# Kernel tuning notes

Measured on AMD Instinct MI355X. Metric: run time of the kernel, lower is better.

Reference implementation:

```python
import jax, jax.numpy as jnp
import numpy as np

B, T, F, U, L = 64, 700, 3, 400, 3


def setup_inputs() -> dict:
    key = jax.random.key(0)
    ks = jax.random.split(key, 10)
    s = 0.08  # small init to keep gates unsaturated
    return {
        "x": jax.random.normal(ks[0], (B, T, F), jnp.float32),
        "Wx0": jax.random.normal(ks[1], (F, 4 * U), jnp.float32) * s,
        "Wx1": jax.random.normal(ks[2], (U, 4 * U), jnp.float32) * s,
        "Wx2": jax.random.normal(ks[3], (U, 4 * U), jnp.float32) * s,
        "Wh": jax.random.normal(ks[4], (L, U, 4 * U), jnp.float32) * s,
        "b": jnp.zeros((L, 4 * U), jnp.float32),
        "pi": jax.random.normal(ks[5], (L, U), jnp.float32) * s,
        "pf": jax.random.normal(ks[6], (L, U), jnp.float32) * s,
        "po": jax.random.normal(ks[7], (L, U), jnp.float32) * s,
        "Wd": jax.random.normal(ks[8], (U, F), jnp.float32) * s,
        "bd": jnp.zeros((F,), jnp.float32),
    }


def _lstm_peephole_layer(x_tbd, Wx, Wh_l, b_l, pi_l, pf_l, po_l):
    """x_tbd: [T, B, D] -> [T, B, U] with peephole LSTM (Graves 2013)."""
    Bsz = x_tbd.shape[1]
    Uu = Wh_l.shape[0]
    # Precompute the input contribution for all timesteps in one GEMM.
    xp = jnp.einsum("tbd,dk->tbk", x_tbd, Wx) + b_l  # [T, B, 4U]

    def step(carry, zt):
        h, c = carry
        z = zt + h @ Wh_l  # [B, 4U]
        zi, zf, zg, zo = jnp.split(z, 4, axis=-1)
        i = jax.nn.sigmoid(zi + pi_l * c)
        f = jax.nn.sigmoid(zf + pf_l * c)
        c_new = f * c + i * jnp.tanh(zg)
        o = jax.nn.sigmoid(zo + po_l * c_new)
        h_new = o * jnp.tanh(c_new)
        return (h_new, c_new), h_new

    init = (jnp.zeros((Bsz, Uu), x_tbd.dtype), jnp.zeros((Bsz, Uu), x_tbd.dtype))
    _, hs = jax.lax.scan(step, init, xp)
    return hs  # [T, B, U]


def reference(x, Wx0, Wx1, Wx2, Wh, b, pi, pf, po, Wd, bd):
    h = jnp.transpose(x, (1, 0, 2))  # [T, B, F]
    for l, Wx in enumerate((Wx0, Wx1, Wx2)):
        h = _lstm_peephole_layer(h, Wx, Wh[l], b[l], pi[l], pf[l], po[l])
    out = jnp.einsum("tbu,uf->tbf", h, Wd) + bd
    return jnp.transpose(out, (1, 0, 2))  # [B, T, F]
```

## Files before the change

### kernel.cpp

```cpp
#include <hip/hip_runtime.h>
#include <hip/hip_fp16.h>
#include <math.h>

#define B_ 64
#define T_ 700
#define U_ 400
#define NF 704
#define FR_LS 13312

typedef _Float16 half8 __attribute__((ext_vector_type(8)));
typedef float float4v __attribute__((ext_vector_type(4)));

union AFrag { unsigned u[4]; half8 h; };

__device__ __forceinline__ unsigned agloadu(const unsigned* p) {
    return __hip_atomic_load(p, __ATOMIC_RELAXED, __HIP_MEMORY_SCOPE_AGENT);
}
__device__ __forceinline__ void agstoreu(unsigned* p, unsigned v) {
    __hip_atomic_store(p, v, __ATOMIC_RELAXED, __HIP_MEMORY_SCOPE_AGENT);
}
__device__ __forceinline__ float sig_(float v) {
    return __builtin_amdgcn_rcpf(1.f + __expf(-v));
}
__device__ __forceinline__ float tanh_(float v) {
    return 1.f - 2.f * __builtin_amdgcn_rcpf(__expf(2.f * v) + 1.f);
}
__device__ __forceinline__ void waitflag(const unsigned* f, unsigned target) {
    while (agloadu(f) < target) __builtin_amdgcn_s_sleep(2);
}
__device__ __forceinline__ unsigned f16u(float v) {
    union { _Float16 f; unsigned short s; } cv; cv.f = (_Float16)v; return (unsigned)cv.s;
}

__device__ __forceinline__ void pollfrag13(const unsigned* __restrict__ base,
                                           const unsigned par,
                                           AFrag* __restrict__ a, const int lane)
{
    {
        const unsigned* pp = base + (lane % 13) * 256 + ((lane * 37) & 255);
        while (!__all((int)(((agloadu(pp) ^ par) & 1u) == 0u)))
            __builtin_amdgcn_s_sleep(3);
    }
    unsigned pend = 0x1FFFu;
    do {
#pragma unroll
        for (int ck = 0; ck < 13; ++ck) if ((pend >> ck) & 1) {
#pragma unroll
            for (int d = 0; d < 4; ++d)
                a[ck].u[d] = agloadu(base + ck * 256 + d * 64 + lane);
        }
#pragma unroll
        for (int ck = 0; ck < 13; ++ck) if ((pend >> ck) & 1) {
            const unsigned m = (a[ck].u[0] ^ par) | (a[ck].u[1] ^ par)
                             | (a[ck].u[2] ^ par) | (a[ck].u[3] ^ par);
            if (__all((int)((m & 1u) == 0u))) pend &= ~(1u << ck);
        }
        if (pend) __builtin_amdgcn_s_sleep(3);
    } while (pend);
}

template<int DEPTH, int CP>
__global__ void __launch_bounds__(256, 1)
lstm_mix(const float* __restrict__ x,
         const float* __restrict__ Wx0,
         const float* __restrict__ Wx1,
         const float* __restrict__ Wx2,
         const float* __restrict__ Wh,
         const float* __restrict__ bias,
         const float* __restrict__ pi,
         const float* __restrict__ pf,
         const float* __restrict__ po,
         const float* __restrict__ Wd,
         const float* __restrict__ bd,
         float* __restrict__ out,
         unsigned* __restrict__ ws)
{
    __shared__ alignas(16) _Float16 wlds[26 * 512];
    __shared__ alignas(16) float zlds[4 * 528];
    __shared__ float gc[160];

    const int LW = NF * CP * 32;
    unsigned* F0 = ws;
    unsigned* F1 = F0 + LW;
    unsigned* F2 = F1 + LW;
    unsigned* FO = F2 + LW;
    unsigned* frag0 = ws + (size_t)4 * LW;

    const int blk  = blockIdx.x;
    const int tid  = threadIdx.x;
    const int lane = tid & 63;
    const int wv   = tid >> 6;
    const int cpi  = (blk + wv) & (CP - 1);

    int layer, u0;
    if      (blk < 50)  { layer = 0; u0 = blk * 8; }
    else if (blk < 150) { layer = 1; u0 = (blk - 50) * 4; }
    else if (blk < 250) { layer = 2; u0 = (blk - 150) * 4; }
    else                { layer = 3; u0 = 0; }

    const bool padw = (blk == 49) || (blk == 149) || (blk == 249);
    int pad_off[2];
    {
        const int i0 = tid, i1 = tid + 256;
        pad_off[0] = (i0 >> 7) * 3328 + 12 * 256 + (((i0 >> 4) & 3) * 64)
                   + (2 + ((i0 >> 6) & 1)) * 16 + (i0 & 15);
        pad_off[1] = (i1 >> 7) * 3328 + 12 * 256 + (((i1 >> 4) & 3) * 64)
                   + (2 + ((i1 >> 6) & 1)) * 16 + (i1 & 15);
    }

    {
        const float* __restrict__ Wxl = (layer == 1) ? Wx1 : Wx2;
        for (int i = tid; i < 26 * 64; i += 256) {
            const int ln = i & 63, ck = i >> 6;
            const int q = ln >> 4, nn = ln & 15;
            float vals[8];
#pragma unroll
            for (int j = 0; j < 8; ++j) {
                const int kc = ck % 13;
                const int k = kc * 32 + q * 8 + j;
                float v = 0.f;
                if (k < 400) {
                    if (layer == 0) {
                        const int col32 = (ck / 13) * 16 + nn;
                        const int gcol = (col32 >> 3) * U_ + u0 + (col32 & 7);
                        v = Wh[(size_t)k * 1600 + gcol];
                    } else if (layer < 3) {
                        const int gcol = (nn >> 2) * U_ + u0 + (nn & 3);
                        v = (ck >= 13) ? Wh[((size_t)layer * U_ + k) * 1600 + gcol]
                                       : Wxl[(size_t)k * 1600 + gcol];
                    } else {
                        if (ck < 13 && nn < 3) v = Wd[k * 3 + nn];
                    }
                }
                vals[j] = v;
            }
#pragma unroll
            for (int j = 0; j < 8; ++j)
                wlds[ck * 512 + ln * 8 + j] = (_Float16)vals[j];
        }
        if (layer == 0) {
            if (tid < 128) {
                const int col32 = tid >> 2, comp = tid & 3;
                const int gcol = (col32 >> 3) * U_ + u0 + (col32 & 7);
                gc[tid] = (comp == 0) ? bias[gcol] : Wx0[(size_t)(comp - 1) * 1600 + gcol];
            } else if (tid < 152) {
                const int idx = tid - 128, ul = idx / 3, j = idx - ul * 3;
                const float* pp = (j == 0) ? pi : (j == 1) ? pf : po;
                gc[tid] = pp[u0 + ul];
            }
        } else if (layer < 3) {
            if (tid < 16) {
                gc[tid] = bias[layer * 1600 + (tid >> 2) * U_ + u0 + (tid & 3)];
            } else if (tid < 28) {
                const int idx = tid - 16, ul = idx / 3, j = idx - ul * 3;
                const float* pp = (j == 0) ? pi : (j == 1) ? pf : po;
                gc[tid] = pp[layer * U_ + u0 + ul];
            }
        } else {
            if (tid < 3) gc[tid] = bd[tid];
        }
    }
    __syncthreads();

    const int wvz   = wv * 528;
    const int b_loc = lane & 15;
    const int quad  = lane >> 4;
    float cst[2] = {0.f, 0.f};

    for (int t = 0; t < T_; ++t) {
        const int sw = t % DEPTH;
        const int sr = (t + DEPTH - 1) % DEPTH;
        const unsigned pI = (unsigned)((t / DEPTH) & 1);
        const unsigned pO = (unsigned)(((t - 1) / DEPTH) & 1);

        float x0, x1, x2;
        if (layer == 0) {
            const size_t xb = (size_t)(wv * 16 + b_loc) * T_ + t;
            x0 = x[xb * 3 + 0]; x1 = x[xb * 3 + 1]; x2 = x[xb * 3 + 2];
        }

        if (lane == 0) {
            if (layer == 0) {
                if (wv == 0 && t >= DEPTH) waitflag(F1 + ((t - DEPTH) * CP + cpi) * 32, 100);
            } else if (layer == 1) {
                waitflag(F0 + (t * CP + cpi) * 32, 50);
                if (wv == 0 && t >= DEPTH) waitflag(F2 + ((t - DEPTH) * CP + cpi) * 32, 100);
            } else if (layer == 2) {
                waitflag(F1 + (t * CP + cpi) * 32, 100);
                if (wv == 0 && t >= DEPTH) waitflag(FO + ((t - DEPTH) * CP + cpi) * 32, 1);
            } else {
                waitflag(F2 + (t * CP + cpi) * 32, 100);
            }
        }
        asm volatile("" ::: "memory");

        AFrag ainp[13];
        if (layer == 1 || layer == 2) {
            const unsigned* frI = frag0 + (size_t)((layer - 1) * DEPTH + sw) * FR_LS + wv * 3328;
#pragma unroll
            for (int kc = 0; kc < 13; ++kc)
#pragma unroll
                for (int d = 0; d < 4; ++d)
                    ainp[kc].u[d] = agloadu(frI + kc * 256 + d * 64 + lane);
        }

        AFrag aown[13];
        if (layer == 3) {
            const unsigned* frI = frag0 + (size_t)(2 * DEPTH + sw) * FR_LS + wv * 3328;
#pragma unroll
            for (int kc = 0; kc < 13; ++kc)
#pragma unroll
                for (int d = 0; d < 4; ++d)
                    aown[kc].u[d] = agloadu(frI + kc * 256 + d * 64 + lane);
        } else if (t >= 1) {
            const unsigned* frO = frag0 + (size_t)(layer * DEPTH + sr) * FR_LS + wv * 3328;
            pollfrag13(frO, pO, aown, lane);
        } else {
#pragma unroll
            for (int kc = 0; kc < 13; ++kc)
#pragma unroll
                for (int d = 0; d < 4; ++d) aown[kc].u[d] = 0u;
        }
        asm volatile("" ::: "memory");

        if (layer == 0) {
            float4v acc0 = {0.f, 0.f, 0.f, 0.f}, acc1 = {0.f, 0.f, 0.f, 0.f};
#pragma unroll
            for (int kc = 0; kc < 13; ++kc) {
                const half8 w0 = *(const half8*)&wlds[kc * 512 + lane * 8];
                const half8 w1 = *(const half8*)&wlds[(13 + kc) * 512 + lane * 8];
                acc0 = __builtin_amdgcn_mfma_f32_16x16x32_f16(aown[kc].h, w0, acc0, 0, 0, 0);
                acc1 = __builtin_amdgcn_mfma_f32_16x16x32_f16(aown[kc].h, w1, acc1, 0, 0, 0);
            }
#pragma unroll
            for (int r = 0; r < 4; ++r) {
                zlds[wvz + (quad * 4 + r) * 33 + b_loc] = acc0[r];
                zlds[wvz + (quad * 4 + r) * 33 + 16 + b_loc] = acc1[r];
            }
        } else if (layer < 3) {
            float4v acc = {0.f, 0.f, 0.f, 0.f};
#pragma unroll
            for (int kc = 0; kc < 13; ++kc) {
                const half8 wA = *(const half8*)&wlds[kc * 512 + lane * 8];
                const half8 wB = *(const half8*)&wlds[(13 + kc) * 512 + lane * 8];
                acc = __builtin_amdgcn_mfma_f32_16x16x32_f16(ainp[kc].h, wA, acc, 0, 0, 0);
                acc = __builtin_amdgcn_mfma_f32_16x16x32_f16(aown[kc].h, wB, acc, 0, 0, 0);
            }
#pragma unroll
            for (int r = 0; r < 4; ++r)
                zlds[wvz + (quad * 4 + r) * 33 + b_loc] = acc[r];
        } else {
            float4v acc = {0.f, 0.f, 0.f, 0.f};
#pragma unroll
            for (int kc = 0; kc < 13; ++kc) {
                const half8 w0 = *(const half8*)&wlds[kc * 512 + lane * 8];
                acc = __builtin_amdgcn_mfma_f32_16x16x32_f16(aown[kc].h, w0, acc, 0, 0, 0);
            }
            if (b_loc < 3) {
#pragma unroll
                for (int r = 0; r < 4; ++r)
                    out[((size_t)(wv * 16 + quad * 4 + r) * T_ + t) * 3 + b_loc] = acc[r] + gc[b_loc];
            }
        }
        __syncthreads();

        if (padw) {
            unsigned* fr_dst = frag0 + (size_t)(layer * DEPTH + sw) * FR_LS;
            agstoreu(fr_dst + pad_off[0], pI);
            agstoreu(fr_dst + pad_off[1], pI);
        }

        if (layer == 0) {
            unsigned* fr_dst = frag0 + (size_t)(0 * DEPTH + sw) * FR_LS + wv * 3328;
#pragma unroll
            for (int q = 0; q < 2; ++q) {
                const int ul = q * 4 + quad;
                const int ug = u0 + ul;
                float z[4];
#pragma unroll
                for (int g = 0; g < 4; ++g) {
                    const int gb = (g * 8 + ul) * 4;
                    z[g] = zlds[wvz + b_loc * 33 + g * 8 + ul]
                         + gc[gb + 0] + x0 * gc[gb + 1] + x1 * gc[gb + 2] + x2 * gc[gb + 3];
                }
                const float cp = cst[q];
                const float ig = sig_(z[0] + gc[128 + ul * 3 + 0] * cp);
                const float fg = sig_(z[1] + gc[128 + ul * 3 + 1] * cp);
                const float cn = fg * cp + ig * tanh_(z[2]);
                const float og = sig_(z[3] + gc[128 + ul * 3 + 2] * cn);
                cst[q] = cn;
                const float hv = og * tanh_(cn);
                const float pv = __shfl_xor(hv, 16, 64);
                if ((quad & 1) == 0) {
                    const unsigned pw_ = ((f16u(hv) & ~1u) | pI) | (f16u(pv) << 16);
                    const int u = ug;
                    agstoreu(fr_dst + (u >> 5) * 256 + ((u & 7) >> 1) * 64
                                    + ((u >> 3) & 3) * 16 + b_loc, pw_);
                }
            }
        } else if (layer < 3) {
            unsigned* fr_dst = frag0 + (size_t)(layer * DEPTH + sw) * FR_LS + wv * 3328;
            const int ul = quad;
            float z[4];
#pragma unroll
            for (int g = 0; g < 4; ++g)
                z[g] = zlds[wvz + b_loc * 33 + g * 4 + ul] + gc[g * 4 + ul];
            const float cp = cst[0];
            const float ig = sig_(z[0] + gc[16 + ul * 3 + 0] * cp);
            const float fg = sig_(z[1] + gc[16 + ul * 3 + 1] * cp);
            const float cn = fg * cp + ig * tanh_(z[2]);
            const float og = sig_(z[3] + gc[16 + ul * 3 + 2] * cn);
            cst[0] = cn;
            const float hv = og * tanh_(cn);
            const float pv = __shfl_xor(hv, 16, 64);
            if ((ul & 1) == 0) {
                const unsigned pw_ = ((f16u(hv) & ~1u) | pI) | (f16u(pv) << 16);
                const int u = u0 + ul;
                agstoreu(fr_dst + (u >> 5) * 256 + ((u & 7) >> 1) * 64
                                + ((u >> 3) & 3) * 16 + b_loc, pw_);
            }
        }

        asm volatile("s_waitcnt vmcnt(0)" ::: "memory");
        __syncthreads();
        if (tid < CP) {
            unsigned* f = (layer == 0) ? F0 : (layer == 1) ? F1
                        : (layer == 2) ? F2 : FO;
            __hip_atomic_fetch_add(f + (t * CP + tid) * 32, 1u,
                                   __ATOMIC_RELAXED, __HIP_MEMORY_SCOPE_AGENT);
        }
    }
}

template<int DEPTH, int CP>
static void launch_variant(void* const* d_in, float* out, unsigned* ws, hipStream_t stream) {
    const float* x    = (const float*)d_in[0];
    const float* Wx0  = (const float*)d_in[1];
    const float* Wx1  = (const float*)d_in[2];
    const float* Wx2  = (const float*)d_in[3];
    const float* Wh   = (const float*)d_in[4];
    const float* bias = (const float*)d_in[5];
    const float* pi   = (const float*)d_in[6];
    const float* pf   = (const float*)d_in[7];
    const float* po   = (const float*)d_in[8];
    const float* Wd   = (const float*)d_in[9];
    const float* bd   = (const float*)d_in[10];
    void* args[] = { (void*)&x, (void*)&Wx0, (void*)&Wx1, (void*)&Wx2, (void*)&Wh,
                     (void*)&bias, (void*)&pi, (void*)&pf, (void*)&po,
                     (void*)&Wd, (void*)&bd, (void*)&out, (void*)&ws };
    hipError_t err = hipLaunchCooperativeKernel((void*)lstm_mix<DEPTH, CP>,
                                                dim3(251), dim3(256), args, 0, stream);
    if (err != hipSuccess)
        hipLaunchKernelGGL((lstm_mix<DEPTH, CP>), dim3(251), dim3(256), 0, stream,
                           x, Wx0, Wx1, Wx2, Wh, bias, pi, pf, po, Wd, bd, out, ws);
}

extern "C" void kernel_launch(void* const* d_in, const int* in_sizes, int n_in,
                              void* d_out, int out_size, void* d_ws, size_t ws_size,
                              hipStream_t stream) {
    float* out = (float*)d_out;
    unsigned* ws = (unsigned*)d_ws;

    auto flagbytes = [](int cp) -> size_t { return (size_t)4 * NF * cp * 32 * 4; };
    auto fragbytes = [](int depth) -> size_t { return (size_t)3 * depth * FR_LS * 4; };

    if (ws_size >= flagbytes(8) + fragbytes(8)) {
        hipMemsetAsync(d_ws, 0, flagbytes(8), stream);
        hipMemsetAsync((char*)d_ws + flagbytes(8), 0xFF, fragbytes(8), stream);
        launch_variant<8, 8>(d_in, out, ws, stream);
    } else if (ws_size >= flagbytes(4) + fragbytes(4)) {
        hipMemsetAsync(d_ws, 0, flagbytes(4), stream);
        hipMemsetAsync((char*)d_ws + flagbytes(4), 0xFF, fragbytes(4), stream);
        launch_variant<4, 4>(d_in, out, ws, stream);
    } else {
        hipMemsetAsync(d_ws, 0, flagbytes(2), stream);
        hipMemsetAsync((char*)d_ws + flagbytes(2), 0xFF, fragbytes(2), stream);
        launch_variant<2, 2>(d_in, out, ws, stream);
    }
}
```

Baseline: 2.852 ms.

## Replace producer-count flag waits with parity-bit polling on input fragments

Consumer layers stop waiting on per-timestep counter flags from the previous layer. Instead they poll the input and recurrent fragments together through parity bits embedded in the fp16 data (pollfrag26). The trailing vmcnt wait, barrier and atomic increment at the end of each step are removed. Layers 1-3 now signal their slot-release counters right after the matmul barrier, so only the back-pressure waits remain. The intent is to cut per-step synchronisation latency on the serial recurrence. The risk is more polling traffic, and possible ordering hazards because the flag increment now comes before the step's own stores.

New measurement: 4.756 ms. +66.7%, slower.

```diff
diff --git a/kernel.cpp b/kernel.cpp
--- a/kernel.cpp
+++ b/kernel.cpp
@@ -36,11 +36,6 @@
                                            const unsigned par,
                                            AFrag* __restrict__ a, const int lane)
 {
-    {
-        const unsigned* pp = base + (lane % 13) * 256 + ((lane * 37) & 255);
-        while (!__all((int)(((agloadu(pp) ^ par) & 1u) == 0u)))
-            __builtin_amdgcn_s_sleep(3);
-    }
     unsigned pend = 0x1FFFu;
     do {
 #pragma unroll
@@ -55,7 +50,42 @@
                              | (a[ck].u[2] ^ par) | (a[ck].u[3] ^ par);
             if (__all((int)((m & 1u) == 0u))) pend &= ~(1u << ck);
         }
-        if (pend) __builtin_amdgcn_s_sleep(3);
+        if (pend) __builtin_amdgcn_s_sleep(2);
+    } while (pend);
+}
+
+__device__ __forceinline__ void pollfrag26(const unsigned* __restrict__ bI, const unsigned parI,
+                                           const unsigned* __restrict__ bO, const unsigned parO,
+                                           AFrag* __restrict__ aI, AFrag* __restrict__ aO,
+                                           const int lane)
+{
+    unsigned pend = 0x03FFFFFFu;
+    do {
+#pragma unroll
+        for (int ck = 0; ck < 13; ++ck) if ((pend >> ck) & 1) {
+#pragma unroll
+            for (int d = 0; d < 4; ++d)
+                aI[ck].u[d] = agloadu(bI + ck * 256 + d * 64 + lane);
+        }
+#pragma unroll
+        for (int ck = 0; ck < 13; ++ck) if ((pend >> (13 + ck)) & 1) {
+#pragma unroll
+            for (int d = 0; d < 4; ++d)
+                aO[ck].u[d] = agloadu(bO + ck * 256 + d * 64 + lane);
+        }
+#pragma unroll
+        for (int ck = 0; ck < 13; ++ck) if ((pend >> ck) & 1) {
+            const unsigned m = (aI[ck].u[0] ^ parI) | (aI[ck].u[1] ^ parI)
+                             | (aI[ck].u[2] ^ parI) | (aI[ck].u[3] ^ parI);
+            if (__all((int)((m & 1u) == 0u))) pend &= ~(1u << ck);
+        }
+#pragma unroll
+        for (int ck = 0; ck < 13; ++ck) if ((pend >> (13 + ck)) & 1) {
+            const unsigned m = (aO[ck].u[0] ^ parO) | (aO[ck].u[1] ^ parO)
+                             | (aO[ck].u[2] ^ parO) | (aO[ck].u[3] ^ parO);
+            if (__all((int)((m & 1u) == 0u))) pend &= ~(1u << (13 + ck));
+        }
+        if (pend) __builtin_amdgcn_s_sleep(2);
     } while (pend);
 }
 
@@ -179,47 +209,40 @@
             x0 = x[xb * 3 + 0]; x1 = x[xb * 3 + 1]; x2 = x[xb * 3 + 2];
         }
 
-        if (lane == 0) {
-            if (layer == 0) {
-                if (wv == 0 && t >= DEPTH) waitflag(F1 + ((t - DEPTH) * CP + cpi) * 32, 100);
-            } else if (layer == 1) {
-                waitflag(F0 + (t * CP + cpi) * 32, 50);
-                if (wv == 0 && t >= DEPTH) waitflag(F2 + ((t - DEPTH) * CP + cpi) * 32, 100);
-            } else if (layer == 2) {
-                waitflag(F1 + (t * CP + cpi) * 32, 100);
-                if (wv == 0 && t >= DEPTH) waitflag(FO + ((t - DEPTH) * CP + cpi) * 32, 1);
+        if (lane == 0 && wv == 0 && t >= DEPTH) {
+            if      (layer == 0) waitflag(F1 + ((t - DEPTH) * CP + cpi) * 32, 100);
+            else if (layer == 1) waitflag(F2 + ((t - DEPTH) * CP + cpi) * 32, 100);
+            else if (layer == 2) waitflag(FO + ((t - DEPTH) * CP + cpi) * 32, 1);
+        }
+        asm volatile("" ::: "memory");
+
+        AFrag ainp[13];
+        AFrag aown[13];
+        if (layer == 0) {
+            if (t >= 1) {
+                const unsigned* frO = frag0 + (size_t)(0 * DEPTH + sr) * FR_LS + wv * 3328;
+                pollfrag13(frO, pO, aown, lane);
             } else {
-                waitflag(F2 + (t * CP + cpi) * 32, 100);
-            }
-        }
-        asm volatile("" ::: "memory");
-
-        AFrag ainp[13];
-        if (layer == 1 || layer == 2) {
+#pragma unroll
+                for (int kc = 0; kc < 13; ++kc)
+#pragma unroll
+                    for (int d = 0; d < 4; ++d) aown[kc].u[d] = 0u;
+            }
+        } else if (layer < 3) {
             const unsigned* frI = frag0 + (size_t)((layer - 1) * DEPTH + sw) * FR_LS + wv * 3328;
-#pragma unroll
-            for (int kc = 0; kc < 13; ++kc)
-#pragma unroll
-                for (int d = 0; d < 4; ++d)
-                    ainp[kc].u[d] = agloadu(frI + kc * 256 + d * 64 + lane);
-        }
-
-        AFrag aown[13];
-        if (layer == 3) {
+            if (t >= 1) {
+                const unsigned* frO = frag0 + (size_t)(layer * DEPTH + sr) * FR_LS + wv * 3328;
+                pollfrag26(frI, pI, frO, pO, ainp, aown, lane);
+            } else {
+                pollfrag13(frI, pI, ainp, lane);
+#pragma unroll
+                for (int kc = 0; kc < 13; ++kc)
+#pragma unroll
+                    for (int d = 0; d < 4; ++d) aown[kc].u[d] = 0u;
+            }
+        } else {
             const unsigned* frI = frag0 + (size_t)(2 * DEPTH + sw) * FR_LS + wv * 3328;
-#pragma unroll
-            for (int kc = 0; kc < 13; ++kc)
-#pragma unroll
-                for (int d = 0; d < 4; ++d)
-                    aown[kc].u[d] = agloadu(frI + kc * 256 + d * 64 + lane);
-        } else if (t >= 1) {
-            const unsigned* frO = frag0 + (size_t)(layer * DEPTH + sr) * FR_LS + wv * 3328;
-            pollfrag13(frO, pO, aown, lane);
-        } else {
-#pragma unroll
-            for (int kc = 0; kc < 13; ++kc)
-#pragma unroll
-                for (int d = 0; d < 4; ++d) aown[kc].u[d] = 0u;
+            pollfrag13(frI, pI, aown, lane);
         }
         asm volatile("" ::: "memory");
 
@@ -268,6 +291,12 @@
             unsigned* fr_dst = frag0 + (size_t)(layer * DEPTH + sw) * FR_LS;
             agstoreu(fr_dst + pad_off[0], pI);
             agstoreu(fr_dst + pad_off[1], pI);
+        }
+
+        if (layer != 0 && tid < CP) {
+            unsigned* f = (layer == 1) ? F1 : (layer == 2) ? F2 : FO;
+            __hip_atomic_fetch_add(f + (t * CP + tid) * 32, 1u,
+                                   __ATOMIC_RELAXED, __HIP_MEMORY_SCOPE_AGENT);
         }
 
         if (layer == 0) {
@@ -319,15 +348,6 @@
                 agstoreu(fr_dst + (u >> 5) * 256 + ((u & 7) >> 1) * 64
                                 + ((u >> 3) & 3) * 16 + b_loc, pw_);
             }
-        }
-
-        asm volatile("s_waitcnt vmcnt(0)" ::: "memory");
-        __syncthreads();
-        if (tid < CP) {
-            unsigned* f = (layer == 0) ? F0 : (layer == 1) ? F1
-                        : (layer == 2) ? F2 : FO;
-            __hip_atomic_fetch_add(f + (t * CP + tid) * 32, 1u,
-                                   __ATOMIC_RELAXED, __HIP_MEMORY_SCOPE_AGENT);
         }
     }
 }
```

## Add XCD-aware persistent LSTM kernel splitting batch into two groups

Applied to the files above, without the earlier changes.

Adds a new cooperative kernel that reads each block's XCC id, assigns roles so that blocks of the same layer and batch half share an XCD, and splits the batch into two independent 32-row groups. Each layer's units are spread over 50 blocks of 128 threads. h fragments are written twice, once with workgroup scope for an L2-local fast poll path via LDS DMA, and once with agent scope as a fallback. The intent is to cut cross-XCD synchronization latency per timestep. The cost is a more complex role assignment, doubled stores, and bounded probing with a sticky fallback.

Measured after the change: 6.850 ms. +140.2%, slower.

```diff
diff --git a/kernel.cpp b/kernel.cpp
--- a/kernel.cpp
+++ b/kernel.cpp
@@ -8,6 +8,15 @@
 #define NF 704
 #define FR_LS 13312
 
+#define XDEP 8
+#define XNB 512
+#define XFRG 6656
+#define XTAB 64
+#define XFLG 1024
+#define XFRAG 2048
+#define PROBE_MAX 1200
+#define VER_MAX 256
+
 typedef _Float16 half8 __attribute__((ext_vector_type(8)));
 typedef float float4v __attribute__((ext_vector_type(4)));
 
@@ -19,6 +28,9 @@
 __device__ __forceinline__ void agstoreu(unsigned* p, unsigned v) {
     __hip_atomic_store(p, v, __ATOMIC_RELAXED, __HIP_MEMORY_SCOPE_AGENT);
 }
+__device__ __forceinline__ void wgstoreu(unsigned* p, unsigned v) {
+    __hip_atomic_store(p, v, __ATOMIC_RELAXED, __HIP_MEMORY_SCOPE_WORKGROUP);
+}
 __device__ __forceinline__ float sig_(float v) {
     return __builtin_amdgcn_rcpf(1.f + __expf(-v));
 }
@@ -27,6 +39,13 @@
 }
 __device__ __forceinline__ void waitflag(const unsigned* f, unsigned target) {
     while (agloadu(f) < target) __builtin_amdgcn_s_sleep(2);
+}
+__device__ __forceinline__ void voteflag(const unsigned* f, unsigned thr, int lane, int nval) {
+    for (;;) {
+        const unsigned v = agloadu(f + lane);
+        if (__all((int)((lane < nval) ? (v >= thr) : 1))) break;
+        __builtin_amdgcn_s_sleep(3);
+    }
 }
 __device__ __forceinline__ unsigned f16u(float v) {
     union { _Float16 f; unsigned short s; } cv; cv.f = (_Float16)v; return (unsigned)cv.s;
@@ -328,6 +347,384 @@
                         : (layer == 2) ? F2 : FO;
             __hip_atomic_fetch_add(f + (t * CP + tid) * 32, 1u,
                                    __ATOMIC_RELAXED, __HIP_MEMORY_SCOPE_AGENT);
+        }
+    }
+}
+
+
+__device__ __forceinline__ void dma4sc0(const unsigned* g, unsigned* l) {
+    __builtin_amdgcn_global_load_lds(
+        (const __attribute__((address_space(1))) void*)g,
+        (__attribute__((address_space(3))) void*)l, 4, 0, 1);
+}
+
+__device__ __forceinline__ bool pollfast(const unsigned* __restrict__ base,
+                                         unsigned* __restrict__ stage,
+                                         unsigned* __restrict__ pb,
+                                         const unsigned par, const int lane,
+                                         AFrag* __restrict__ a)
+{
+    {
+        const unsigned* pp = base + (lane % 13) * 256 + ((lane * 37) & 255);
+        int it = 0;
+        for (;;) {
+            dma4sc0(pp, pb);
+            asm volatile("s_waitcnt vmcnt(0)" ::: "memory");
+            __builtin_amdgcn_sched_barrier(0);
+            const unsigned v = *(volatile unsigned*)&pb[lane];
+            if (__all((int)(((v ^ par) & 1u) == 0u))) break;
+            if (++it >= PROBE_MAX) return false;
+            __builtin_amdgcn_s_sleep(1);
+        }
+    }
+    unsigned pend = 0x1FFFu;
+    int it = 0;
+    do {
+#pragma unroll
+        for (int ck = 0; ck < 13; ++ck) if ((pend >> ck) & 1) {
+#pragma unroll
+            for (int d = 0; d < 4; ++d)
+                dma4sc0(base + ck * 256 + d * 64 + lane, stage + ck * 256 + d * 64);
+        }
+        asm volatile("s_waitcnt vmcnt(0)" ::: "memory");
+        __builtin_amdgcn_sched_barrier(0);
+#pragma unroll
+        for (int ck = 0; ck < 13; ++ck) if ((pend >> ck) & 1) {
+#pragma unroll
+            for (int d = 0; d < 4; ++d)
+                a[ck].u[d] = *(volatile unsigned*)&stage[ck * 256 + d * 64 + lane];
+            const unsigned m = (a[ck].u[0] ^ par) | (a[ck].u[1] ^ par)
+                             | (a[ck].u[2] ^ par) | (a[ck].u[3] ^ par);
+            if (__all((int)((m & 1u) == 0u))) pend &= ~(1u << ck);
+        }
+        if (pend) {
+            if (++it >= VER_MAX) return false;
+            __builtin_amdgcn_s_sleep(1);
+        }
+    } while (pend);
+    return true;
+}
+
+__global__ void __launch_bounds__(128, 1)
+lstm_xcd(const float* __restrict__ x,
+         const float* __restrict__ Wx0,
+         const float* __restrict__ Wx1,
+         const float* __restrict__ Wx2,
+         const float* __restrict__ Wh,
+         const float* __restrict__ bias,
+         const float* __restrict__ pi,
+         const float* __restrict__ pf,
+         const float* __restrict__ po,
+         const float* __restrict__ Wd,
+         const float* __restrict__ bd,
+         float* __restrict__ out,
+         unsigned* __restrict__ ws)
+{
+    __shared__ alignas(16) unsigned shbuf[13312];
+    __shared__ alignas(16) float zlds[1056];
+    __shared__ unsigned problds[128];
+    __shared__ float gc[160];
+    __shared__ unsigned shmisc[2];
+
+    const int blk  = blockIdx.x;
+    const int tid  = threadIdx.x;
+    const int lane = tid & 63;
+    const int wv   = tid >> 6;
+
+    if (tid == 0) {
+        unsigned xcc = 0;
+        asm volatile("s_getreg_b32 %0, hwreg(20, 0, 32)" : "=s"(xcc));
+        shmisc[0] = xcc & 15u;
+        agstoreu(ws + XTAB + blk, xcc & 15u);
+        __hip_atomic_fetch_add(ws, 1u, __ATOMIC_RELEASE, __HIP_MEMORY_SCOPE_AGENT);
+        while (__hip_atomic_load(ws, __ATOMIC_ACQUIRE, __HIP_MEMORY_SCOPE_AGENT)
+               < (unsigned)gridDim.x)
+            __builtin_amdgcn_s_sleep(7);
+    }
+    __syncthreads();
+
+    if (tid == 0) {
+        const int myx = (int)shmisc[0];
+        int cnt[16];
+#pragma unroll
+        for (int i = 0; i < 16; ++i) cnt[i] = 0;
+        int rank = 0;
+        for (int j = 0; j < (int)gridDim.x; ++j) {
+            const int xj = (int)(agloadu(ws + XTAB + j) & 15u);
+            if (xj == myx && j < blk) ++rank;
+            ++cnt[xj];
+        }
+        int mx = 0;
+        for (int i = 0; i < 16; ++i) if (cnt[i] > mx) mx = cnt[i];
+        const int need6[6] = {50, 50, 51, 50, 50, 51};
+        const int base6[6] = {0, 50, 100, 151, 201, 251};
+        int rem[16];
+#pragma unroll
+        for (int i = 0; i < 16; ++i) rem[i] = cnt[i];
+        int setx[6];
+        bool valid = (mx <= 100);
+        for (int s = 0; s < 6; ++s) {
+            int best = 0;
+            for (int xx = 1; xx < 16; ++xx) if (rem[xx] > rem[best]) best = xx;
+            if (rem[best] < need6[s]) valid = false;
+            setx[s] = best; rem[best] -= need6[s];
+        }
+        int role = -1;
+        if (valid) {
+            int acc = 0;
+            for (int s = 0; s < 6; ++s) if (setx[s] == myx) {
+                if (role < 0 && rank >= acc && rank < acc + need6[s])
+                    role = base6[s] + (rank - acc);
+                acc += need6[s];
+            }
+        } else if (blk < 302) role = blk;
+        shmisc[0] = (unsigned)(role + 1);
+        shmisc[1] = valid ? 1u : 0u;
+    }
+    __syncthreads();
+    const int role = (int)shmisc[0] - 1;
+    const bool l2ok = shmisc[1] != 0;
+    if (role < 0) return;
+
+    const int grp = (role >= 151) ? 1 : 0;
+    const int r   = role - grp * 151;
+    int layer, rk;
+    if      (r < 50)  { layer = 0; rk = r; }
+    else if (r < 100) { layer = 1; rk = r - 50; }
+    else if (r < 150) { layer = 2; rk = r - 100; }
+    else              { layer = 3; rk = 0; }
+    const int u0 = rk * 8;
+    const bool padw = (rk == 49) && (layer < 3);
+
+    unsigned* flg = ws + XFLG + grp * 256;
+    auto regp = [&](int which, int slot) -> unsigned* {
+        return ws + XFRAG + (size_t)((grp * 6 + which) * XDEP + slot) * XFRG;
+    };
+
+    {
+        const int TCH = (layer == 0) ? 26 : (layer < 3) ? 52 : 13;
+        const float* __restrict__ Wxl = (layer == 1) ? Wx1 : Wx2;
+        _Float16* wldsh = (_Float16*)shbuf;
+        for (int i = tid; i < TCH * 64; i += 128) {
+            const int ln = i & 63, ck = i >> 6;
+            const int q = ln >> 4, nn = ln & 15;
+            float vals[8];
+#pragma unroll
+            for (int j = 0; j < 8; ++j) {
+                float v = 0.f;
+                if (layer == 3) {
+                    const int k = ck * 32 + q * 8 + j;
+                    if (k < 400 && nn < 3) v = Wd[k * 3 + nn];
+                } else if (layer == 0) {
+                    const int col32 = (ck / 13) * 16 + nn;
+                    const int gcol = (col32 >> 3) * U_ + u0 + (col32 & 7);
+                    const int k = (ck % 13) * 32 + q * 8 + j;
+                    if (k < 400) v = Wh[(size_t)k * 1600 + gcol];
+                } else {
+                    const int tile = ck / 26, ck2 = ck % 26;
+                    const int col32 = tile * 16 + nn;
+                    const int gcol = (col32 >> 3) * U_ + u0 + (col32 & 7);
+                    const int kc13 = (ck2 < 13) ? ck2 : (ck2 - 13);
+                    const int k = kc13 * 32 + q * 8 + j;
+                    if (k < 400) v = (ck2 < 13) ? Wxl[(size_t)k * 1600 + gcol]
+                                                : Wh[((size_t)layer * U_ + k) * 1600 + gcol];
+                }
+                vals[j] = v;
+            }
+#pragma unroll
+            for (int j = 0; j < 8; ++j) wldsh[ck * 512 + ln * 8 + j] = (_Float16)vals[j];
+        }
+        if (layer == 0) {
+            if (tid < 128) {
+                const int col32 = tid >> 2, comp = tid & 3;
+                const int gcol = (col32 >> 3) * U_ + u0 + (col32 & 7);
+                gc[tid] = (comp == 0) ? bias[gcol] : Wx0[(size_t)(comp - 1) * 1600 + gcol];
+            }
+            if (tid < 24) {
+                const int ul = tid / 3, j = tid - ul * 3;
+                const float* pp = (j == 0) ? pi : (j == 1) ? pf : po;
+                gc[128 + tid] = pp[u0 + ul];
+            }
+        } else if (layer < 3) {
+            if (tid < 32) gc[tid] = bias[layer * 1600 + (tid >> 3) * U_ + u0 + (tid & 7)];
+            if (tid < 24) {
+                const int ul = tid / 3, j = tid - ul * 3;
+                const float* pp = (j == 0) ? pi : (j == 1) ? pf : po;
+                gc[32 + tid] = pp[layer * U_ + u0 + ul];
+            }
+        } else {
+            if (tid < 3) gc[tid] = bd[tid];
+        }
+    }
+    __syncthreads();
+    half8 bfr[52];
+    {
+        const _Float16* wldsh = (const _Float16*)shbuf;
+#pragma unroll
+        for (int ck = 0; ck < 52; ++ck)
+            bfr[ck] = *(const half8*)&wldsh[ck * 512 + lane * 8];
+    }
+    __syncthreads();
+
+    unsigned* stage = shbuf + wv * 3328;
+    unsigned* pb    = problds + wv * 64;
+    const int wvz   = wv * 528;
+    const int b_loc = lane & 15;
+    const int quad  = lane >> 4;
+    float cst[2] = {0.f, 0.f};
+    int sticky = l2ok ? 0 : 1;
+
+    for (int t = 0; t < T_; ++t) {
+        const int sw = t % XDEP;
+        const int sr = (t + XDEP - 1) % XDEP;
+        const unsigned pI = (unsigned)((t / XDEP) & 1);
+        const unsigned pO = (unsigned)(((t - 1) / XDEP) & 1);
+
+        float x0, x1, x2;
+        if (layer == 0) {
+            const size_t xb = (size_t)(grp * 32 + wv * 16 + b_loc) * T_ + t;
+            x0 = x[xb * 3 + 0]; x1 = x[xb * 3 + 1]; x2 = x[xb * 3 + 2];
+        }
+
+        if (wv == 0 && t >= XDEP) {
+            if      (layer == 0) voteflag(flg + 64,  (unsigned)(t - XDEP + 1), lane, 50);
+            else if (layer == 1) voteflag(flg + 128, (unsigned)(t - XDEP + 1), lane, 50);
+            else if (layer == 2) { if (lane == 0) waitflag(flg + 192, (unsigned)(t - XDEP + 1)); }
+        }
+        asm volatile("" ::: "memory");
+
+        AFrag ainp[13];
+        if (layer == 1 || layer == 2) {
+            voteflag(flg + (layer - 1) * 64, (unsigned)(t + 1), lane, 50);
+            asm volatile("" ::: "memory");
+            const unsigned* frI = regp(2 * (layer - 1) + 1, sw) + wv * 3328;
+#pragma unroll
+            for (int kc = 0; kc < 13; ++kc)
+#pragma unroll
+                for (int d = 0; d < 4; ++d)
+                    ainp[kc].u[d] = agloadu(frI + kc * 256 + d * 64 + lane);
+        }
+
+        AFrag aown[13];
+        if (layer == 3) {
+            bool ok = false;
+            if (!sticky) {
+                ok = pollfast(regp(4, sw) + wv * 3328, stage, pb, pI, lane, aown);
+                if (!ok) sticky = 1;
+            }
+            if (!ok) pollfrag13(regp(5, sw) + wv * 3328, pI, aown, lane);
+        } else if (t >= 1) {
+            bool ok = false;
+            if (!sticky) {
+                ok = pollfast(regp(2 * layer, sr) + wv * 3328, stage, pb, pO, lane, aown);
+                if (!ok) sticky = 1;
+            }
+            if (!ok) pollfrag13(regp(2 * layer + 1, sr) + wv * 3328, pO, aown, lane);
+        } else {
+#pragma unroll
+            for (int kc = 0; kc < 13; ++kc)
+#pragma unroll
+                for (int d = 0; d < 4; ++d) aown[kc].u[d] = 0u;
+        }
+        asm volatile("" ::: "memory");
+
+        if (layer == 0) {
+            float4v acc0 = {0.f, 0.f, 0.f, 0.f}, acc1 = {0.f, 0.f, 0.f, 0.f};
+#pragma unroll
+            for (int kc = 0; kc < 13; ++kc) {
+                acc0 = __builtin_amdgcn_mfma_f32_16x16x32_f16(aown[kc].h, bfr[kc], acc0, 0, 0, 0);
+                acc1 = __builtin_amdgcn_mfma_f32_16x16x32_f16(aown[kc].h, bfr[13 + kc], acc1, 0, 0, 0);
+            }
+#pragma unroll
+            for (int r2 = 0; r2 < 4; ++r2) {
+                zlds[wvz + (quad * 4 + r2) * 33 + b_loc] = acc0[r2];
+                zlds[wvz + (quad * 4 + r2) * 33 + 16 + b_loc] = acc1[r2];
+            }
+        } else if (layer < 3) {
+            float4v acc0 = {0.f, 0.f, 0.f, 0.f}, acc1 = {0.f, 0.f, 0.f, 0.f};
+#pragma unroll
+            for (int kc = 0; kc < 13; ++kc) {
+                acc0 = __builtin_amdgcn_mfma_f32_16x16x32_f16(ainp[kc].h, bfr[kc], acc0, 0, 0, 0);
+                acc0 = __builtin_amdgcn_mfma_f32_16x16x32_f16(aown[kc].h, bfr[13 + kc], acc0, 0, 0, 0);
+                acc1 = __builtin_amdgcn_mfma_f32_16x16x32_f16(ainp[kc].h, bfr[26 + kc], acc1, 0, 0, 0);
+                acc1 = __builtin_amdgcn_mfma_f32_16x16x32_f16(aown[kc].h, bfr[39 + kc], acc1, 0, 0, 0);
+            }
+#pragma unroll
+            for (int r2 = 0; r2 < 4; ++r2) {
+                zlds[wvz + (quad * 4 + r2) * 33 + b_loc] = acc0[r2];
+                zlds[wvz + (quad * 4 + r2) * 33 + 16 + b_loc] = acc1[r2];
+            }
+        } else {
+            float4v acc0 = {0.f, 0.f, 0.f, 0.f};
+#pragma unroll
+            for (int kc = 0; kc < 13; ++kc)
+                acc0 = __builtin_amdgcn_mfma_f32_16x16x32_f16(aown[kc].h, bfr[kc], acc0, 0, 0, 0);
+            if (b_loc < 3) {
+#pragma unroll
+                for (int r2 = 0; r2 < 4; ++r2)
+                    out[((size_t)(grp * 32 + wv * 16 + quad * 4 + r2) * T_ + t) * 3 + b_loc]
+                        = acc0[r2] + gc[b_loc];
+            }
+        }
+        __syncthreads();
+
+        if (padw) {
+            unsigned* pP = regp(2 * layer, sw);
+            unsigned* pX = regp(2 * layer + 1, sw);
+#pragma unroll
+            for (int s2 = 0; s2 < 2; ++s2) {
+                const int i = tid + s2 * 128;
+                const int off = (i >> 7) * 3328 + 12 * 256 + (((i >> 5) & 3) * 64)
+                              + (2 + ((i >> 4) & 1)) * 16 + (i & 15);
+                wgstoreu(pP + off, pI);
+                agstoreu(pX + off, pI);
+            }
+        }
+
+        if (layer < 3) {
+            unsigned* dstP = regp(2 * layer, sw) + wv * 3328;
+            unsigned* dstX = regp(2 * layer + 1, sw) + wv * 3328;
+            const float* pe = (layer == 0) ? (gc + 128) : (gc + 32);
+#pragma unroll
+            for (int q = 0; q < 2; ++q) {
+                const int ul = q * 4 + quad;
+                const int ug = u0 + ul;
+                float z[4];
+                if (layer == 0) {
+#pragma unroll
+                    for (int gt = 0; gt < 4; ++gt) {
+                        const int gb = (gt * 8 + ul) * 4;
+                        z[gt] = zlds[wvz + b_loc * 33 + gt * 8 + ul]
+                              + gc[gb + 0] + x0 * gc[gb + 1] + x1 * gc[gb + 2] + x2 * gc[gb + 3];
+                    }
+                } else {
+#pragma unroll
+                    for (int gt = 0; gt < 4; ++gt)
+                        z[gt] = zlds[wvz + b_loc * 33 + gt * 8 + ul] + gc[gt * 8 + ul];
+                }
+                const float cp = cst[q];
+                const float ig = sig_(z[0] + pe[ul * 3 + 0] * cp);
+                const float fg = sig_(z[1] + pe[ul * 3 + 1] * cp);
+                const float cn = fg * cp + ig * tanh_(z[2]);
+                const float og = sig_(z[3] + pe[ul * 3 + 2] * cn);
+                cst[q] = cn;
+                const float hv = og * tanh_(cn);
+                const float pv = __shfl_xor(hv, 16, 64);
+                if ((quad & 1) == 0) {
+                    const unsigned pw_ = ((f16u(hv) & ~1u) | pI) | (f16u(pv) << 16);
+                    const int off = (ug >> 5) * 256 + ((ug & 7) >> 1) * 64
+                                  + ((ug >> 3) & 3) * 16 + b_loc;
+                    wgstoreu(dstP + off, pw_);
+                    agstoreu(dstX + off, pw_);
+                }
+            }
+        }
+
+        asm volatile("s_waitcnt vmcnt(0)" ::: "memory");
+        __syncthreads();
+        if (tid == 0) {
+            if (layer < 3) agstoreu(flg + layer * 64 + rk, (unsigned)(t + 1));
+            else           agstoreu(flg + 192, (unsigned)(t + 1));
         }
     }
 }
@@ -361,6 +758,30 @@
     float* out = (float*)d_out;
     unsigned* ws = (unsigned*)d_ws;
 
+    const size_t xcd_need = ((size_t)XFRAG + (size_t)2 * 6 * XDEP * XFRG) * 4;
+    if (ws_size >= xcd_need) {
+        hipMemsetAsync(d_ws, 0, (size_t)XFRAG * 4, stream);
+        hipMemsetAsync((char*)d_ws + (size_t)XFRAG * 4, 0xFF,
+                       (size_t)2 * 6 * XDEP * XFRG * 4, stream);
+        const float* x    = (const float*)d_in[0];
+        const float* Wx0  = (const float*)d_in[1];
+        const float* Wx1  = (const float*)d_in[2];
+        const float* Wx2  = (const float*)d_in[3];
+        const float* Wh   = (const float*)d_in[4];
+        const float* bias = (const float*)d_in[5];
+        const float* pi   = (const float*)d_in[6];
+        const float* pf   = (const float*)d_in[7];
+        const float* po   = (const float*)d_in[8];
+        const float* Wd   = (const float*)d_in[9];
+        const float* bd   = (const float*)d_in[10];
+        void* args[] = { (void*)&x, (void*)&Wx0, (void*)&Wx1, (void*)&Wx2, (void*)&Wh,
+                         (void*)&bias, (void*)&pi, (void*)&pf, (void*)&po,
+                         (void*)&Wd, (void*)&bd, (void*)&out, (void*)&ws };
+        hipError_t err = hipLaunchCooperativeKernel((void*)lstm_xcd,
+                                                    dim3(XNB), dim3(128), args, 0, stream);
+        if (err == hipSuccess) return;
+    }
+
     auto flagbytes = [](int cp) -> size_t { return (size_t)4 * NF * cp * 32 * 4; };
     auto fragbytes = [](int depth) -> size_t { return (size_t)3 * depth * FR_LS * 4; };
 
```

## Halve blocks for layers 1-2 and replace atomic counters with per-block flag slots

Applied to the files above, without the earlier changes.

Layers 1 and 2 now use 50 blocks of 8 units each instead of 100 blocks of 4, so each block runs two MFMA accumulator tiles and the gate math is shared with layer 0. The grid drops from 251 to 151 blocks. The atomic-increment counters are replaced by per-producer flag words, which consumers check with a wave-wide vote over 64 lanes, and the replica count is reduced. This aims to cut the number of blocks taking part in synchronisation and the contention on shared atomic counters, at the cost of twice the per-block compute and LDS weight storage in the middle layers.

Measured after the change: 3.350 ms. 1.17x slower.

```diff
diff --git a/kernel.cpp b/kernel.cpp
--- a/kernel.cpp
+++ b/kernel.cpp
@@ -25,11 +25,16 @@
 __device__ __forceinline__ float tanh_(float v) {
     return 1.f - 2.f * __builtin_amdgcn_rcpf(__expf(2.f * v) + 1.f);
 }
-__device__ __forceinline__ void waitflag(const unsigned* f, unsigned target) {
-    while (agloadu(f) < target) __builtin_amdgcn_s_sleep(2);
-}
 __device__ __forceinline__ unsigned f16u(float v) {
     union { _Float16 f; unsigned short s; } cv; cv.f = (_Float16)v; return (unsigned)cv.s;
+}
+
+__device__ __forceinline__ void votenz(const unsigned* f, const int lane, const int nval) {
+    for (;;) {
+        const unsigned v = agloadu(f + lane);
+        if (__all((int)((lane < nval) ? (v != 0u) : 1))) break;
+        __builtin_amdgcn_s_sleep(2);
+    }
 }
 
 __device__ __forceinline__ void pollfrag13(const unsigned* __restrict__ base,
@@ -59,27 +64,27 @@
     } while (pend);
 }
 
-template<int DEPTH, int CP>
+template<int DEPTH, int REP>
 __global__ void __launch_bounds__(256, 1)
-lstm_mix(const float* __restrict__ x,
-         const float* __restrict__ Wx0,
-         const float* __restrict__ Wx1,
-         const float* __restrict__ Wx2,
-         const float* __restrict__ Wh,
-         const float* __restrict__ bias,
-         const float* __restrict__ pi,
-         const float* __restrict__ pf,
-         const float* __restrict__ po,
-         const float* __restrict__ Wd,
-         const float* __restrict__ bd,
-         float* __restrict__ out,
-         unsigned* __restrict__ ws)
+lstm_mix2(const float* __restrict__ x,
+          const float* __restrict__ Wx0,
+          const float* __restrict__ Wx1,
+          const float* __restrict__ Wx2,
+          const float* __restrict__ Wh,
+          const float* __restrict__ bias,
+          const float* __restrict__ pi,
+          const float* __restrict__ pf,
+          const float* __restrict__ po,
+          const float* __restrict__ Wd,
+          const float* __restrict__ bd,
+          float* __restrict__ out,
+          unsigned* __restrict__ ws)
 {
-    __shared__ alignas(16) _Float16 wlds[26 * 512];
+    __shared__ alignas(16) _Float16 wlds[52 * 512];
     __shared__ alignas(16) float zlds[4 * 528];
     __shared__ float gc[160];
 
-    const int LW = NF * CP * 32;
+    const int LW = NF * REP * 64;
     unsigned* F0 = ws;
     unsigned* F1 = F0 + LW;
     unsigned* F2 = F1 + LW;
@@ -90,15 +95,16 @@
     const int tid  = threadIdx.x;
     const int lane = tid & 63;
     const int wv   = tid >> 6;
-    const int cpi  = (blk + wv) & (CP - 1);
-
-    int layer, u0;
-    if      (blk < 50)  { layer = 0; u0 = blk * 8; }
-    else if (blk < 150) { layer = 1; u0 = (blk - 50) * 4; }
-    else if (blk < 250) { layer = 2; u0 = (blk - 150) * 4; }
-    else                { layer = 3; u0 = 0; }
-
-    const bool padw = (blk == 49) || (blk == 149) || (blk == 249);
+    const int rep  = (blk + wv) & (REP - 1);
+
+    int layer, rk;
+    if      (blk < 50)  { layer = 0; rk = blk; }
+    else if (blk < 100) { layer = 1; rk = blk - 50; }
+    else if (blk < 150) { layer = 2; rk = blk - 100; }
+    else                { layer = 3; rk = 0; }
+    const int u0 = rk * 8;
+
+    const bool padw = (blk == 49) || (blk == 99) || (blk == 149);
     int pad_off[2];
     {
         const int i0 = tid, i1 = tid + 256;
@@ -110,27 +116,30 @@
 
     {
         const float* __restrict__ Wxl = (layer == 1) ? Wx1 : Wx2;
-        for (int i = tid; i < 26 * 64; i += 256) {
+        const int TCH = (layer == 0) ? 26 : (layer < 3) ? 52 : 13;
+        for (int i = tid; i < TCH * 64; i += 256) {
             const int ln = i & 63, ck = i >> 6;
             const int q = ln >> 4, nn = ln & 15;
             float vals[8];
 #pragma unroll
             for (int j = 0; j < 8; ++j) {
-                const int kc = ck % 13;
-                const int k = kc * 32 + q * 8 + j;
                 float v = 0.f;
-                if (k < 400) {
-                    if (layer == 0) {
-                        const int col32 = (ck / 13) * 16 + nn;
-                        const int gcol = (col32 >> 3) * U_ + u0 + (col32 & 7);
-                        v = Wh[(size_t)k * 1600 + gcol];
-                    } else if (layer < 3) {
-                        const int gcol = (nn >> 2) * U_ + u0 + (nn & 3);
-                        v = (ck >= 13) ? Wh[((size_t)layer * U_ + k) * 1600 + gcol]
-                                       : Wxl[(size_t)k * 1600 + gcol];
-                    } else {
-                        if (ck < 13 && nn < 3) v = Wd[k * 3 + nn];
-                    }
+                if (layer == 0) {
+                    const int col32 = (ck / 13) * 16 + nn;
+                    const int gcol = (col32 >> 3) * U_ + u0 + (col32 & 7);
+                    const int k = (ck % 13) * 32 + q * 8 + j;
+                    if (k < 400) v = Wh[(size_t)k * 1600 + gcol];
+                } else if (layer < 3) {
+                    const int tile = ck / 26, ck2 = ck % 26;
+                    const int col32 = tile * 16 + nn;
+                    const int gcol = (col32 >> 3) * U_ + u0 + (col32 & 7);
+                    const int kc13 = (ck2 < 13) ? ck2 : (ck2 - 13);
+                    const int k = kc13 * 32 + q * 8 + j;
+                    if (k < 400) v = (ck2 < 13) ? Wxl[(size_t)k * 1600 + gcol]
+                                                : Wh[((size_t)layer * U_ + k) * 1600 + gcol];
+                } else {
+                    const int k = ck * 32 + q * 8 + j;
+                    if (k < 400 && nn < 3) v = Wd[k * 3 + nn];
                 }
                 vals[j] = v;
             }
@@ -149,12 +158,11 @@
                 gc[tid] = pp[u0 + ul];
             }
         } else if (layer < 3) {
-            if (tid < 16) {
-                gc[tid] = bias[layer * 1600 + (tid >> 2) * U_ + u0 + (tid & 3)];
-            } else if (tid < 28) {
-                const int idx = tid - 16, ul = idx / 3, j = idx - ul * 3;
+            if (tid < 32) gc[tid] = bias[layer * 1600 + (tid >> 3) * U_ + u0 + (tid & 7)];
+            else if (tid < 56) {
+                const int idx = tid - 32, ul = idx / 3, j = idx - ul * 3;
                 const float* pp = (j == 0) ? pi : (j == 1) ? pf : po;
-                gc[tid] = pp[layer * U_ + u0 + ul];
+                gc[32 + idx] = pp[layer * U_ + u0 + ul];
             }
         } else {
             if (tid < 3) gc[tid] = bd[tid];
@@ -179,18 +187,19 @@
             x0 = x[xb * 3 + 0]; x1 = x[xb * 3 + 1]; x2 = x[xb * 3 + 2];
         }
 
-        if (lane == 0) {
-            if (layer == 0) {
-                if (wv == 0 && t >= DEPTH) waitflag(F1 + ((t - DEPTH) * CP + cpi) * 32, 100);
-            } else if (layer == 1) {
-                waitflag(F0 + (t * CP + cpi) * 32, 50);
-                if (wv == 0 && t >= DEPTH) waitflag(F2 + ((t - DEPTH) * CP + cpi) * 32, 100);
-            } else if (layer == 2) {
-                waitflag(F1 + (t * CP + cpi) * 32, 100);
-                if (wv == 0 && t >= DEPTH) waitflag(FO + ((t - DEPTH) * CP + cpi) * 32, 1);
-            } else {
-                waitflag(F2 + (t * CP + cpi) * 32, 100);
-            }
+        if (layer == 0) {
+            if (wv == 0 && t >= DEPTH)
+                votenz(F1 + ((size_t)(t - DEPTH) * REP + rep) * 64, lane, 50);
+        } else if (layer == 1) {
+            votenz(F0 + ((size_t)t * REP + rep) * 64, lane, 50);
+            if (wv == 0 && t >= DEPTH)
+                votenz(F2 + ((size_t)(t - DEPTH) * REP + rep) * 64, lane, 50);
+        } else if (layer == 2) {
+            votenz(F1 + ((size_t)t * REP + rep) * 64, lane, 50);
+            if (wv == 0 && t >= DEPTH)
+                votenz(FO + ((size_t)(t - DEPTH) * REP + rep) * 64, lane, 1);
+        } else {
+            votenz(F2 + ((size_t)t * REP + rep) * 64, lane, 50);
         }
         asm volatile("" ::: "memory");
 
@@ -238,17 +247,23 @@
                 zlds[wvz + (quad * 4 + r) * 33 + 16 + b_loc] = acc1[r];
             }
         } else if (layer < 3) {
-            float4v acc = {0.f, 0.f, 0.f, 0.f};
+            float4v acc0 = {0.f, 0.f, 0.f, 0.f}, acc1 = {0.f, 0.f, 0.f, 0.f};
 #pragma unroll
             for (int kc = 0; kc < 13; ++kc) {
-                const half8 wA = *(const half8*)&wlds[kc * 512 + lane * 8];
-                const half8 wB = *(const half8*)&wlds[(13 + kc) * 512 + lane * 8];
-                acc = __builtin_amdgcn_mfma_f32_16x16x32_f16(ainp[kc].h, wA, acc, 0, 0, 0);
-                acc = __builtin_amdgcn_mfma_f32_16x16x32_f16(aown[kc].h, wB, acc, 0, 0, 0);
-            }
-#pragma unroll
-            for (int r = 0; r < 4; ++r)
-                zlds[wvz + (quad * 4 + r) * 33 + b_loc] = acc[r];
+                const half8 wA0 = *(const half8*)&wlds[kc * 512 + lane * 8];
+                const half8 wB0 = *(const half8*)&wlds[(13 + kc) * 512 + lane * 8];
+                const half8 wA1 = *(const half8*)&wlds[(26 + kc) * 512 + lane * 8];
+                const half8 wB1 = *(const half8*)&wlds[(39 + kc) * 512 + lane * 8];
+                acc0 = __builtin_amdgcn_mfma_f32_16x16x32_f16(ainp[kc].h, wA0, acc0, 0, 0, 0);
+                acc0 = __builtin_amdgcn_mfma_f32_16x16x32_f16(aown[kc].h, wB0, acc0, 0, 0, 0);
+                acc1 = __builtin_amdgcn_mfma_f32_16x16x32_f16(ainp[kc].h, wA1, acc1, 0, 0, 0);
+                acc1 = __builtin_amdgcn_mfma_f32_16x16x32_f16(aown[kc].h, wB1, acc1, 0, 0, 0);
+            }
+#pragma unroll
+            for (int r = 0; r < 4; ++r) {
+                zlds[wvz + (quad * 4 + r) * 33 + b_loc] = acc0[r];
+                zlds[wvz + (quad * 4 + r) * 33 + 16 + b_loc] = acc1[r];
+            }
         } else {
             float4v acc = {0.f, 0.f, 0.f, 0.f};
 #pragma unroll
@@ -270,24 +285,31 @@
             agstoreu(fr_dst + pad_off[1], pI);
         }
 
-        if (layer == 0) {
-            unsigned* fr_dst = frag0 + (size_t)(0 * DEPTH + sw) * FR_LS + wv * 3328;
+        if (layer < 3) {
+            unsigned* fr_dst = frag0 + (size_t)(layer * DEPTH + sw) * FR_LS + wv * 3328;
+            const float* pe = (layer == 0) ? (gc + 128) : (gc + 32);
 #pragma unroll
             for (int q = 0; q < 2; ++q) {
                 const int ul = q * 4 + quad;
                 const int ug = u0 + ul;
                 float z[4];
-#pragma unroll
-                for (int g = 0; g < 4; ++g) {
-                    const int gb = (g * 8 + ul) * 4;
-                    z[g] = zlds[wvz + b_loc * 33 + g * 8 + ul]
-                         + gc[gb + 0] + x0 * gc[gb + 1] + x1 * gc[gb + 2] + x2 * gc[gb + 3];
+                if (layer == 0) {
+#pragma unroll
+                    for (int g = 0; g < 4; ++g) {
+                        const int gb = (g * 8 + ul) * 4;
+                        z[g] = zlds[wvz + b_loc * 33 + g * 8 + ul]
+                             + gc[gb + 0] + x0 * gc[gb + 1] + x1 * gc[gb + 2] + x2 * gc[gb + 3];
+                    }
+                } else {
+#pragma unroll
+                    for (int g = 0; g < 4; ++g)
+                        z[g] = zlds[wvz + b_loc * 33 + g * 8 + ul] + gc[g * 8 + ul];
                 }
                 const float cp = cst[q];
-                const float ig = sig_(z[0] + gc[128 + ul * 3 + 0] * cp);
-                const float fg = sig_(z[1] + gc[128 + ul * 3 + 1] * cp);
+                const float ig = sig_(z[0] + pe[ul * 3 + 0] * cp);
+                const float fg = sig_(z[1] + pe[ul * 3 + 1] * cp);
                 const float cn = fg * cp + ig * tanh_(z[2]);
-                const float og = sig_(z[3] + gc[128 + ul * 3 + 2] * cn);
+                const float og = sig_(z[3] + pe[ul * 3 + 2] * cn);
                 cst[q] = cn;
                 const float hv = og * tanh_(cn);
                 const float pv = __shfl_xor(hv, 16, 64);
@@ -298,41 +320,19 @@
                                     + ((u >> 3) & 3) * 16 + b_loc, pw_);
                 }
             }
-        } else if (layer < 3) {
-            unsigned* fr_dst = frag0 + (size_t)(layer * DEPTH + sw) * FR_LS + wv * 3328;
-            const int ul = quad;
-            float z[4];
-#pragma unroll
-            for (int g = 0; g < 4; ++g)
-                z[g] = zlds[wvz + b_loc * 33 + g * 4 + ul] + gc[g * 4 + ul];
-            const float cp = cst[0];
-            const float ig = sig_(z[0] + gc[16 + ul * 3 + 0] * cp);
-            const float fg = sig_(z[1] + gc[16 + ul * 3 + 1] * cp);
-            const float cn = fg * cp + ig * tanh_(z[2]);
-            const float og = sig_(z[3] + gc[16 + ul * 3 + 2] * cn);
-            cst[0] = cn;
-            const float hv = og * tanh_(cn);
-            const float pv = __shfl_xor(hv, 16, 64);
-            if ((ul & 1) == 0) {
-                const unsigned pw_ = ((f16u(hv) & ~1u) | pI) | (f16u(pv) << 16);
-                const int u = u0 + ul;
-                agstoreu(fr_dst + (u >> 5) * 256 + ((u & 7) >> 1) * 64
-                                + ((u >> 3) & 3) * 16 + b_loc, pw_);
-            }
         }
 
         asm volatile("s_waitcnt vmcnt(0)" ::: "memory");
         __syncthreads();
-        if (tid < CP) {
+        if (tid < REP) {
             unsigned* f = (layer == 0) ? F0 : (layer == 1) ? F1
                         : (layer == 2) ? F2 : FO;
-            __hip_atomic_fetch_add(f + (t * CP + tid) * 32, 1u,
-                                   __ATOMIC_RELAXED, __HIP_MEMORY_SCOPE_AGENT);
-        }
-    }
-}
-
-template<int DEPTH, int CP>
+            agstoreu(f + ((size_t)t * REP + tid) * 64 + rk, 1u);
+        }
+    }
+}
+
+template<int DEPTH, int REP>
 static void launch_variant(void* const* d_in, float* out, unsigned* ws, hipStream_t stream) {
     const float* x    = (const float*)d_in[0];
     const float* Wx0  = (const float*)d_in[1];
@@ -348,10 +348,10 @@
     void* args[] = { (void*)&x, (void*)&Wx0, (void*)&Wx1, (void*)&Wx2, (void*)&Wh,
                      (void*)&bias, (void*)&pi, (void*)&pf, (void*)&po,
                      (void*)&Wd, (void*)&bd, (void*)&out, (void*)&ws };
-    hipError_t err = hipLaunchCooperativeKernel((void*)lstm_mix<DEPTH, CP>,
-                                                dim3(251), dim3(256), args, 0, stream);
+    hipError_t err = hipLaunchCooperativeKernel((void*)lstm_mix2<DEPTH, REP>,
+                                                dim3(151), dim3(256), args, 0, stream);
     if (err != hipSuccess)
-        hipLaunchKernelGGL((lstm_mix<DEPTH, CP>), dim3(251), dim3(256), 0, stream,
+        hipLaunchKernelGGL((lstm_mix2<DEPTH, REP>), dim3(151), dim3(256), 0, stream,
                            x, Wx0, Wx1, Wx2, Wh, bias, pi, pf, po, Wd, bd, out, ws);
 }
 
@@ -361,20 +361,20 @@
     float* out = (float*)d_out;
     unsigned* ws = (unsigned*)d_ws;
 
-    auto flagbytes = [](int cp) -> size_t { return (size_t)4 * NF * cp * 32 * 4; };
+    auto flagbytes = [](int rep) -> size_t { return (size_t)4 * NF * rep * 64 * 4; };
     auto fragbytes = [](int depth) -> size_t { return (size_t)3 * depth * FR_LS * 4; };
 
-    if (ws_size >= flagbytes(8) + fragbytes(8)) {
-        hipMemsetAsync(d_ws, 0, flagbytes(8), stream);
-        hipMemsetAsync((char*)d_ws + flagbytes(8), 0xFF, fragbytes(8), stream);
-        launch_variant<8, 8>(d_in, out, ws, stream);
-    } else if (ws_size >= flagbytes(4) + fragbytes(4)) {
+    if (ws_size >= flagbytes(4) + fragbytes(8)) {
         hipMemsetAsync(d_ws, 0, flagbytes(4), stream);
-        hipMemsetAsync((char*)d_ws + flagbytes(4), 0xFF, fragbytes(4), stream);
-        launch_variant<4, 4>(d_in, out, ws, stream);
+        hipMemsetAsync((char*)d_ws + flagbytes(4), 0xFF, fragbytes(8), stream);
+        launch_variant<8, 4>(d_in, out, ws, stream);
+    } else if (ws_size >= flagbytes(2) + fragbytes(4)) {
+        hipMemsetAsync(d_ws, 0, flagbytes(2), stream);
+        hipMemsetAsync((char*)d_ws + flagbytes(2), 0xFF, fragbytes(4), stream);
+        launch_variant<4, 2>(d_in, out, ws, stream);
     } else {
-        hipMemsetAsync(d_ws, 0, flagbytes(2), stream);
-        hipMemsetAsync((char*)d_ws + flagbytes(2), 0xFF, fragbytes(2), stream);
-        launch_variant<2, 2>(d_in, out, ws, stream);
-    }
-}
+        hipMemsetAsync(d_ws, 0, flagbytes(1), stream);
+        hipMemsetAsync((char*)d_ws + flagbytes(1), 0xFF, fragbytes(2), stream);
+        launch_variant<2, 1>(d_in, out, ws, stream);
+    }
+}
```
